# Performance work log

Hardware: AMD Instinct MI355X
Metric: run time of the kernel (lower is better)

## Reference

```python
import jax, jax.numpy as jnp
import numpy as np

NDET = 16
N_UP = 8  # spin_split=2 with nelec=16 -> (8, 8)


def _orbitals(s, r, W, b, pi, a):
    """FermiNet orbital layer for one spin.

    s: (B, n, d) backflow stream, r: (B, n, nion, 3) electron-ion displacements,
    W: (d, n*NDET), b: (n*NDET,), pi/a: (nion, n*NDET).
    Returns (NDET, B, n, n) square orbital matrices.
    """
    lin = s @ W + b                                   # (B, n, n*NDET)
    dist = jnp.linalg.norm(r, axis=-1)                # (B, n, nion)
    # isotropic envelope: sum_ion pi[ion, orb] * exp(-a[ion, orb] * |r - R_ion|)
    env = jnp.sum(pi * jnp.exp(-a * dist[..., None]), axis=-2)  # (B, n, n*NDET)
    orb = lin * env
    n = orb.shape[-2]
    orb = orb.reshape(*orb.shape[:-1], NDET, n)       # (B, n, NDET, n)
    return jnp.moveaxis(orb, -2, 0)                   # (NDET, B, n, n)


def setup_inputs() -> dict:
    key = jax.random.key(0)
    ks = jax.random.split(key, 10)
    B, NE, D, NION = 4096, 16, 256, 4
    no = N_UP * NDET
    sc = 1.0 / np.sqrt(D)
    return {
        "stream_1e": jax.random.normal(ks[0], (B, NE, D), jnp.float32),
        "r_ei": jax.random.normal(ks[1], (B, NE, NION, 3), jnp.float32),
        "W_up": jax.random.normal(ks[2], (D, no), jnp.float32) * sc,
        "b_up": jax.random.normal(ks[3], (no,), jnp.float32) * 0.01,
        "pi_up": jax.random.normal(ks[4], (NION, no), jnp.float32),
        "a_up": jax.random.uniform(ks[5], (NION, no), jnp.float32, 0.5, 1.5),
        "W_dn": jax.random.normal(ks[6], (D, no), jnp.float32) * sc,
        "b_dn": jax.random.normal(ks[7], (no,), jnp.float32) * 0.01,
        "pi_dn": jax.random.normal(ks[8], (NION, no), jnp.float32),
        "a_dn": jax.random.uniform(ks[9], (NION, no), jnp.float32, 0.5, 1.5),
    }


def reference(stream_1e, r_ei, W_up, b_up, pi_up, a_up, W_dn, b_dn, pi_dn, a_dn):
    s_up, s_dn = stream_1e[:, :N_UP], stream_1e[:, N_UP:]
    r_up, r_dn = r_ei[:, :N_UP], r_ei[:, N_UP:]
    orb_u = _orbitals(s_up, r_up, W_up, b_up, pi_up, a_up)  # (NDET, B, 8, 8)
    orb_d = _orbitals(s_dn, r_dn, W_dn, b_dn, pi_dn, a_dn)
    sgn_u, log_u = jnp.linalg.slogdet(orb_u)                # (NDET, B)
    sgn_d, log_d = jnp.linalg.slogdet(orb_d)
    sign = sgn_u * sgn_d
    logd = log_u + log_d
    # psi = sum_i det_u_i * det_d_i  (PARALLEL_EVEN, determinant_fn=None)
    m = jnp.max(logd, axis=0)                               # (B,)
    ssum = jnp.sum(sign * jnp.exp(logd - m), axis=0)        # (B,)
    log_psi = m + jnp.log(jnp.abs(ssum))                    # (B,)
    return log_psi
```

## Files before the change

kernel.cpp:

```cpp
#include <hip/hip_runtime.h>
#include <math.h>

#define DD 256
#define NO 128
#define ORW 132
#define ORB_WAVE (32*ORW)
#define UNI_US 33792
#define BUF_US 16384

typedef __attribute__((ext_vector_type(8))) short bf16x8;
typedef __attribute__((ext_vector_type(4))) float f32x4;

static __device__ inline unsigned short f2bf(float x) {
    unsigned int u = __float_as_uint(x);
    unsigned int r = (u + 0x7FFFu + ((u >> 16) & 1u)) >> 16;
    return (unsigned short)r;
}
static __device__ inline float bf2f(unsigned short h) {
    return __uint_as_float(((unsigned int)h) << 16);
}

static __device__ __forceinline__ void gl_lds16(const void* g, void* l) {
    __builtin_amdgcn_global_load_lds(
        (const __attribute__((address_space(1))) void*)g,
        (__attribute__((address_space(3))) void*)l, 16, 0, 0);
}

__global__ void prep_wt3(const float* __restrict__ Wu, const float* __restrict__ Wd,
                         unsigned short* __restrict__ wt3) {
    const int n    = blockIdx.x & 127;
    const int spin = blockIdx.x >> 7;
    const float* W = spin ? Wd : Wu;
    const int t = threadIdx.x;
    for (int k = t; k < DD; k += 64) {
        const float x = W[(size_t)k * NO + n];
        const unsigned short h = f2bf(x);
        const unsigned short l = f2bf(x - bf2f(h));
        const int kt = k >> 5, slot = (k >> 3) & 3, j = k & 7;
        const int rh = spin * 128 + n;
        const int rl = 256 + rh;
        wt3[(size_t)kt * 16384 + rh * 32 + ((slot + rh) & 3) * 8 + j] = h;
        wt3[(size_t)kt * 16384 + rl * 32 + ((slot + rl) & 3) * 8 + j] = l;
    }
}

__global__ __launch_bounds__(256, 2)
void fermi_main(const float* __restrict__ stream1e, const float* __restrict__ r_ei,
                const float* __restrict__ bu, const float* __restrict__ piu,
                const float* __restrict__ au, const float* __restrict__ bd,
                const float* __restrict__ pid_, const float* __restrict__ ad,
                const unsigned short* __restrict__ wt, float* __restrict__ out)
{
    __shared__ __align__(16) unsigned short uni[UNI_US];
    __shared__ __align__(16) float distL[4 * 32 * 4];
    __shared__ float exL[2 * 8 * 16 * 2];

    float* orb = (float*)uni;

    const int t    = threadIdx.x;
    const int w    = t >> 6;
    const int lane = t & 63;
    const int lr   = lane & 15;
    const int lg   = lane >> 4;
    const int sp   = w >> 1;
    const int bh   = w & 1;
    const int b0   = blockIdx.x * 8;

    #pragma unroll
    for (int i = 0; i < 2; ++i) {
        const int idx = lane * 2 + i;
        const int row = idx >> 2, ion = idx & 3;
        const int b  = b0 + bh * 4 + (row >> 3);
        const int ge = sp * 8 + (row & 7);
        const float* rp = r_ei + (((size_t)b * 16 + ge) * 4 + ion) * 3;
        const float x = rp[0], y = rp[1], z = rp[2];
        distL[(w * 32 + row) * 4 + ion] = sqrtf(x * x + y * y + z * z);
    }

    size_t arow0, arow1;
    {
        const int r0 = lr;
        const int r1 = 16 + lr;
        arow0 = (((size_t)(b0 + bh * 4 + (r0 >> 3)) * 16) + sp * 8 + (r0 & 7)) * DD;
        arow1 = (((size_t)(b0 + bh * 4 + (r1 >> 3)) * 16) + sp * 8 + (r1 & 7)) * DD;
    }

    auto stage = [&](int buf, int kt) {
        const unsigned short* gsrc = wt + (size_t)kt * 16384 + w * 4096 + lane * 8;
        unsigned short* ldst = uni + buf * BUF_US + w * 4096;
        #pragma unroll
        for (int i = 0; i < 8; ++i)
            gl_lds16(gsrc + i * 512, ldst + i * 512);
    };

    f32x4 acc[2][8];
    #pragma unroll
    for (int mt = 0; mt < 2; ++mt)
        #pragma unroll
        for (int nt = 0; nt < 8; ++nt)
            acc[mt][nt] = (f32x4){0.f, 0.f, 0.f, 0.f};

    stage(0, 0);
    __syncthreads();

    #pragma unroll
    for (int kt = 0; kt < 8; ++kt) {
        const int cur = kt & 1;
        if (kt < 7) stage(cur ^ 1, kt + 1);

        const int k0 = kt * 32;
        bf16x8 ah[2], al[2];
        #pragma unroll
        for (int mt = 0; mt < 2; ++mt) {
            const float* ap = stream1e + (mt ? arow1 : arow0) + k0 + lg * 8;
            const float4 v0 = *(const float4*)ap;
            const float4 v1 = *(const float4*)(ap + 4);
            const float f[8] = {v0.x, v0.y, v0.z, v0.w, v1.x, v1.y, v1.z, v1.w};
            int hw[4], lw[4];
            #pragma unroll
            for (int p = 0; p < 4; ++p) {
                unsigned int hp;
                asm("v_cvt_pk_bf16_f32 %0, %1, %2" : "=v"(hp) : "v"(f[2*p]), "v"(f[2*p+1]));
                const float h0 = __uint_as_float(hp << 16);
                const float h1 = __uint_as_float(hp & 0xFFFF0000u);
                const float l0 = f[2*p]   - h0;
                const float l1 = f[2*p+1] - h1;
                unsigned int lp;
                asm("v_cvt_pk_bf16_f32 %0, %1, %2" : "=v"(lp) : "v"(l0), "v"(l1));
                hw[p] = (int)hp;
                lw[p] = (int)lp;
            }
            ah[mt] = *(const bf16x8*)hw;
            al[mt] = *(const bf16x8*)lw;
        }
        const unsigned short* bufp = uni + cur * BUF_US;
        const int rot = ((lg + lr) & 3) * 8;
        #pragma unroll
        for (int nt = 0; nt < 8; ++nt) {
            const int rhi = sp * 128 + nt * 16 + lr;
            const bf16x8 bh_ = *(const bf16x8*)(bufp + rhi * 32 + rot);
            const bf16x8 bl_ = *(const bf16x8*)(bufp + 8192 + rhi * 32 + rot);
            acc[0][nt] = __builtin_amdgcn_mfma_f32_16x16x32_bf16(ah[0], bh_, acc[0][nt], 0, 0, 0);
            acc[0][nt] = __builtin_amdgcn_mfma_f32_16x16x32_bf16(ah[0], bl_, acc[0][nt], 0, 0, 0);
            acc[0][nt] = __builtin_amdgcn_mfma_f32_16x16x32_bf16(al[0], bh_, acc[0][nt], 0, 0, 0);
            acc[1][nt] = __builtin_amdgcn_mfma_f32_16x16x32_bf16(ah[1], bh_, acc[1][nt], 0, 0, 0);
            acc[1][nt] = __builtin_amdgcn_mfma_f32_16x16x32_bf16(ah[1], bl_, acc[1][nt], 0, 0, 0);
            acc[1][nt] = __builtin_amdgcn_mfma_f32_16x16x32_bf16(al[1], bh_, acc[1][nt], 0, 0, 0);
        }
        __syncthreads();
    }

    const float* pi_s = sp ? pid_ : piu;
    const float* a_s  = sp ? ad   : au;
    const float* b_s  = sp ? bd   : bu;
    float* ow = orb + (size_t)w * ORB_WAVE;
    {
        float dq[2][4][4];
        #pragma unroll
        for (int mt = 0; mt < 2; ++mt)
            #pragma unroll
            for (int q = 0; q < 4; ++q) {
                const int row = mt * 16 + lg * 4 + q;
                const f32x4 dv = *(const f32x4*)&distL[(w * 32 + row) * 4];
                dq[mt][q][0] = dv[0]; dq[mt][q][1] = dv[1];
                dq[mt][q][2] = dv[2]; dq[mt][q][3] = dv[3];
            }
        #pragma unroll
        for (int nt = 0; nt < 8; ++nt) {
            const int C = nt * 16 + lr;
            float pv[4], av[4];
            #pragma unroll
            for (int ion = 0; ion < 4; ++ion) {
                pv[ion] = pi_s[ion * NO + C];
                av[ion] = a_s [ion * NO + C];
            }
            const float bias = b_s[C];
            #pragma unroll
            for (int mt = 0; mt < 2; ++mt)
                #pragma unroll
                for (int q = 0; q < 4; ++q) {
                    float env = 0.f;
                    #pragma unroll
                    for (int ion = 0; ion < 4; ++ion)
                        env += pv[ion] * __expf(-av[ion] * dq[mt][q][ion]);
                    ow[(mt * 16 + lg * 4 + q) * ORW + C] = (acc[mt][nt][q] + bias) * env;
                }
        }
    }

    {
        const int bl_ = lane >> 4;
        const int dd  = lane & 15;
        const int rot = (lane >> 2) & 7;
        float M[8][8];
        #pragma unroll
        for (int j = 0; j < 8; ++j) {
            const int e = (j + rot) & 7;
            const float* pr = ow + (bl_ * 8 + e) * ORW + dd * 8;
            const f32x4 u0 = *(const f32x4*)pr;
            const f32x4 u1 = *(const f32x4*)(pr + 4);
            M[j][0] = u0[0]; M[j][1] = u0[1]; M[j][2] = u0[2]; M[j][3] = u0[3];
            M[j][4] = u1[0]; M[j][5] = u1[1]; M[j][6] = u1[2]; M[j][7] = u1[3];
        }
        float ldet = 0.f, sgn = (rot & 1) ? -1.f : 1.f;
        #pragma unroll
        for (int c = 0; c < 8; ++c) {
            #pragma unroll
            for (int r = c + 1; r < 8; ++r) {
                const bool swp = fabsf(M[r][c]) > fabsf(M[c][c]);
                sgn = swp ? -sgn : sgn;
                #pragma unroll
                for (int j = c; j < 8; ++j) {
                    const float x1 = M[c][j], x2 = M[r][j];
                    M[c][j] = swp ? x2 : x1;
                    M[r][j] = swp ? x1 : x2;
                }
            }
            const float p = M[c][c];
            ldet += __logf(fabsf(p));
            sgn  = (p < 0.f) ? -sgn : sgn;
            const float rp = (p != 0.f) ? (1.0f / p) : 0.f;
            #pragma unroll
            for (int r = c + 1; r < 8; ++r) {
                const float fm = M[r][c] * rp;
                #pragma unroll
                for (int j = c + 1; j < 8; ++j)
                    M[r][j] = fmaf(-fm, M[c][j], M[r][j]);
            }
        }
        const int bb = bh * 4 + bl_;
        exL[((sp * 8 + bb) * 16 + dd) * 2 + 0] = ldet;
        exL[((sp * 8 + bb) * 16 + dd) * 2 + 1] = sgn;
    }
    __syncthreads();

    if (t < 128) {
        const int b  = t >> 4;
        const int d2 = t & 15;
        const float lu  = exL[((b)     * 16 + d2) * 2 + 0];
        const float su  = exL[((b)     * 16 + d2) * 2 + 1];
        const float ldn = exL[((8 + b) * 16 + d2) * 2 + 0];
        const float sdn = exL[((8 + b) * 16 + d2) * 2 + 1];
        const float l   = lu + ldn;
        const float s   = su * sdn;
        float m = l;
        #pragma unroll
        for (int off = 1; off <= 8; off <<= 1) m = fmaxf(m, __shfl_xor(m, off));
        float ss = s * __expf(l - m);
        #pragma unroll
        for (int off = 1; off <= 8; off <<= 1) ss += __shfl_xor(ss, off);
        if (d2 == 0) out[b0 + b] = m + __logf(fabsf(ss));
    }
}

extern "C" void kernel_launch(void* const* d_in, const int* in_sizes, int n_in,
                              void* d_out, int out_size, void* d_ws, size_t ws_size,
                              hipStream_t stream) {
    (void)n_in; (void)in_sizes; (void)ws_size;
    const float* s1e  = (const float*)d_in[0];
    const float* r_ei = (const float*)d_in[1];
    const float* Wu   = (const float*)d_in[2];
    const float* bu   = (const float*)d_in[3];
    const float* piu  = (const float*)d_in[4];
    const float* au   = (const float*)d_in[5];
    const float* Wd   = (const float*)d_in[6];
    const float* bd   = (const float*)d_in[7];
    const float* pid_ = (const float*)d_in[8];
    const float* ad   = (const float*)d_in[9];
    float* out = (float*)d_out;
    unsigned short* wt3 = (unsigned short*)d_ws;

    hipLaunchKernelGGL(prep_wt3, dim3(256), dim3(64), 0, stream, Wu, Wd, wt3);

    const int B = out_size;
    hipLaunchKernelGGL(fermi_main, dim3(B / 8), dim3(256), 0, stream,
                       s1e, r_ei, bu, piu, au, bd, pid_, ad, wt3, out);
}
```

Before: 37.09 us.

## Split fused kernel into GEMM/envelope kernel and separate determinant kernel

Splits the single fused kernel in two. The first kernel does the bf16-split GEMM and envelope and writes the orbital matrices to a global workspace. The second kernel loads them and runs the 8x8 LU slogdet and logsumexp reduction. This removes the large LDS orbital staging buffer, which could raise occupancy of the GEMM kernel and ease register pressure. In exchange it adds a global write and read of about 32 MB of orbitals plus an extra launch.

Result: slower. 42.43 us (+14.4%).

```diff
diff --git a/kernel.cpp b/kernel.cpp
--- a/kernel.cpp
+++ b/kernel.cpp
@@ -3,10 +3,8 @@
 
 #define DD 256
 #define NO 128
-#define ORW 132
-#define ORB_WAVE (32*ORW)
-#define UNI_US 33792
 #define BUF_US 16384
+#define ORB_OFF (1u << 20)
 
 typedef __attribute__((ext_vector_type(8))) short bf16x8;
 typedef __attribute__((ext_vector_type(4))) float f32x4;
@@ -45,17 +43,14 @@
 }
 
 __global__ __launch_bounds__(256, 2)
-void fermi_main(const float* __restrict__ stream1e, const float* __restrict__ r_ei,
+void fermi_gemm(const float* __restrict__ stream1e, const float* __restrict__ r_ei,
                 const float* __restrict__ bu, const float* __restrict__ piu,
                 const float* __restrict__ au, const float* __restrict__ bd,
                 const float* __restrict__ pid_, const float* __restrict__ ad,
-                const unsigned short* __restrict__ wt, float* __restrict__ out)
+                const unsigned short* __restrict__ wt, float* __restrict__ orb_g)
 {
-    __shared__ __align__(16) unsigned short uni[UNI_US];
+    __shared__ __align__(16) unsigned short uni[2 * BUF_US];
     __shared__ __align__(16) float distL[4 * 32 * 4];
-    __shared__ float exL[2 * 8 * 16 * 2];
-
-    float* orb = (float*)uni;
 
     const int t    = threadIdx.x;
     const int w    = t >> 6;
@@ -153,7 +148,6 @@
     const float* pi_s = sp ? pid_ : piu;
     const float* a_s  = sp ? ad   : au;
     const float* b_s  = sp ? bd   : bu;
-    float* ow = orb + (size_t)w * ORB_WAVE;
     {
         float dq[2][4][4];
         #pragma unroll
@@ -179,59 +173,68 @@
             for (int mt = 0; mt < 2; ++mt)
                 #pragma unroll
                 for (int q = 0; q < 4; ++q) {
+                    const int row = mt * 16 + lg * 4 + q;
+                    const int b   = b0 + bh * 4 + (row >> 3);
+                    const int ge  = sp * 8 + (row & 7);
                     float env = 0.f;
                     #pragma unroll
                     for (int ion = 0; ion < 4; ++ion)
                         env += pv[ion] * __expf(-av[ion] * dq[mt][q][ion]);
-                    ow[(mt * 16 + lg * 4 + q) * ORW + C] = (acc[mt][nt][q] + bias) * env;
+                    orb_g[((size_t)b * 16 + ge) * NO + C] = (acc[mt][nt][q] + bias) * env;
                 }
         }
     }
-
-    {
-        const int bl_ = lane >> 4;
-        const int dd  = lane & 15;
-        const int rot = (lane >> 2) & 7;
-        float M[8][8];
-        #pragma unroll
-        for (int j = 0; j < 8; ++j) {
-            const int e = (j + rot) & 7;
-            const float* pr = ow + (bl_ * 8 + e) * ORW + dd * 8;
-            const f32x4 u0 = *(const f32x4*)pr;
-            const f32x4 u1 = *(const f32x4*)(pr + 4);
-            M[j][0] = u0[0]; M[j][1] = u0[1]; M[j][2] = u0[2]; M[j][3] = u0[3];
-            M[j][4] = u1[0]; M[j][5] = u1[1]; M[j][6] = u1[2]; M[j][7] = u1[3];
-        }
-        float ldet = 0.f, sgn = (rot & 1) ? -1.f : 1.f;
-        #pragma unroll
-        for (int c = 0; c < 8; ++c) {
-            #pragma unroll
-            for (int r = c + 1; r < 8; ++r) {
-                const bool swp = fabsf(M[r][c]) > fabsf(M[c][c]);
-                sgn = swp ? -sgn : sgn;
-                #pragma unroll
-                for (int j = c; j < 8; ++j) {
-                    const float x1 = M[c][j], x2 = M[r][j];
-                    M[c][j] = swp ? x2 : x1;
-                    M[r][j] = swp ? x1 : x2;
-                }
-            }
-            const float p = M[c][c];
-            ldet += __logf(fabsf(p));
-            sgn  = (p < 0.f) ? -sgn : sgn;
-            const float rp = (p != 0.f) ? (1.0f / p) : 0.f;
-            #pragma unroll
-            for (int r = c + 1; r < 8; ++r) {
-                const float fm = M[r][c] * rp;
-                #pragma unroll
-                for (int j = c + 1; j < 8; ++j)
-                    M[r][j] = fmaf(-fm, M[c][j], M[r][j]);
-            }
-        }
-        const int bb = bh * 4 + bl_;
-        exL[((sp * 8 + bb) * 16 + dd) * 2 + 0] = ldet;
-        exL[((sp * 8 + bb) * 16 + dd) * 2 + 1] = sgn;
-    }
+}
+
+__global__ __launch_bounds__(256)
+void fermi_det(const float* __restrict__ orb_g, float* __restrict__ out)
+{
+    __shared__ float exL[2 * 8 * 16 * 2];
+
+    const int t  = threadIdx.x;
+    const int b0 = blockIdx.x * 8;
+    const int bb = t >> 5;
+    const int sub = t & 31;
+    const int sp = sub >> 4;
+    const int dd = sub & 15;
+
+    const float* base = orb_g + (((size_t)(b0 + bb) * 16) + sp * 8) * NO + dd * 8;
+    float M[8][8];
+    #pragma unroll
+    for (int e = 0; e < 8; ++e) {
+        const f32x4 u0 = *(const f32x4*)(base + e * NO);
+        const f32x4 u1 = *(const f32x4*)(base + e * NO + 4);
+        M[e][0] = u0[0]; M[e][1] = u0[1]; M[e][2] = u0[2]; M[e][3] = u0[3];
+        M[e][4] = u1[0]; M[e][5] = u1[1]; M[e][6] = u1[2]; M[e][7] = u1[3];
+    }
+    float ldet = 0.f, sgn = 1.f;
+    #pragma unroll
+    for (int c = 0; c < 8; ++c) {
+        #pragma unroll
+        for (int r = c + 1; r < 8; ++r) {
+            const bool swp = fabsf(M[r][c]) > fabsf(M[c][c]);
+            sgn = swp ? -sgn : sgn;
+            #pragma unroll
+            for (int j = c; j < 8; ++j) {
+                const float x1 = M[c][j], x2 = M[r][j];
+                M[c][j] = swp ? x2 : x1;
+                M[r][j] = swp ? x1 : x2;
+            }
+        }
+        const float p = M[c][c];
+        ldet += __logf(fabsf(p));
+        sgn  = (p < 0.f) ? -sgn : sgn;
+        const float rp = (p != 0.f) ? (1.0f / p) : 0.f;
+        #pragma unroll
+        for (int r = c + 1; r < 8; ++r) {
+            const float fm = M[r][c] * rp;
+            #pragma unroll
+            for (int j = c + 1; j < 8; ++j)
+                M[r][j] = fmaf(-fm, M[c][j], M[r][j]);
+        }
+    }
+    exL[((sp * 8 + bb) * 16 + dd) * 2 + 0] = ldet;
+    exL[((sp * 8 + bb) * 16 + dd) * 2 + 1] = sgn;
     __syncthreads();
 
     if (t < 128) {
@@ -269,10 +272,12 @@
     const float* ad   = (const float*)d_in[9];
     float* out = (float*)d_out;
     unsigned short* wt3 = (unsigned short*)d_ws;
+    float* orb_g = (float*)d_ws + ORB_OFF;
 
     hipLaunchKernelGGL(prep_wt3, dim3(256), dim3(64), 0, stream, Wu, Wd, wt3);
 
     const int B = out_size;
-    hipLaunchKernelGGL(fermi_main, dim3(B / 8), dim3(256), 0, stream,
-                       s1e, r_ei, bu, piu, au, bd, pid_, ad, wt3, out);
-}
+    hipLaunchKernelGGL(fermi_gemm, dim3(B / 8), dim3(256), 0, stream,
+                       s1e, r_ei, bu, piu, au, bd, pid_, ad, wt3, orb_g);
+    hipLaunchKernelGGL(fermi_det, dim3(B / 8), dim3(256), 0, stream, orb_g, out);
+}
```

## Triple-buffer hi weight tiles, read lo weights from global, prefetch activations

Applied to the files above, without the earlier changes.

Only the high-bf16 weight half is staged into LDS now, using a three-deep ring with counted vmcnt waits and raw barriers in place of a full double buffer with __syncthreads. The low-bf16 half is laid out in fragment order and loaded straight from global memory. Activation rows for the next k-step are prefetched into registers one iteration ahead, and MFMA priority is raised around the compute loop. The aim is to shrink LDS traffic and hide load latency, at the cost of more direct global/L2 reads and tight vmcnt bookkeeping that must match the number of loads in flight.

Result: slower. 40.47 us (+9.1%).

```diff
diff --git a/kernel.cpp b/kernel.cpp
--- a/kernel.cpp
+++ b/kernel.cpp
@@ -6,7 +6,8 @@
 #define ORW 132
 #define ORB_WAVE (32*ORW)
 #define UNI_US 33792
-#define BUF_US 16384
+#define TILE_US 8192
+#define LO_OFF 65536
 
 typedef __attribute__((ext_vector_type(8))) short bf16x8;
 typedef __attribute__((ext_vector_type(4))) float f32x4;
@@ -26,21 +27,22 @@
         (__attribute__((address_space(3))) void*)l, 16, 0, 0);
 }
 
-__global__ void prep_wt3(const float* __restrict__ Wu, const float* __restrict__ Wd,
-                         unsigned short* __restrict__ wt3) {
+__global__ void prep_wt4(const float* __restrict__ Wu, const float* __restrict__ Wd,
+                         unsigned short* __restrict__ wt4) {
     const int n    = blockIdx.x & 127;
     const int spin = blockIdx.x >> 7;
     const float* W = spin ? Wd : Wu;
     const int t = threadIdx.x;
+    const int nt = n >> 4, lr = n & 15;
     for (int k = t; k < DD; k += 64) {
         const float x = W[(size_t)k * NO + n];
         const unsigned short h = f2bf(x);
         const unsigned short l = f2bf(x - bf2f(h));
         const int kt = k >> 5, slot = (k >> 3) & 3, j = k & 7;
-        const int rh = spin * 128 + n;
-        const int rl = 256 + rh;
-        wt3[(size_t)kt * 16384 + rh * 32 + ((slot + rh) & 3) * 8 + j] = h;
-        wt3[(size_t)kt * 16384 + rl * 32 + ((slot + rl) & 3) * 8 + j] = l;
+        const int row = spin * 128 + n;
+        wt4[(size_t)kt * TILE_US + row * 32 + ((slot + row) & 3) * 8 + j] = h;
+        wt4[(size_t)LO_OFF + ((size_t)(spin * 8 + kt) * 8 + nt) * 512
+            + (slot * 16 + lr) * 8 + j] = l;
     }
 }
 
@@ -86,10 +88,10 @@
     }
 
     auto stage = [&](int buf, int kt) {
-        const unsigned short* gsrc = wt + (size_t)kt * 16384 + w * 4096 + lane * 8;
-        unsigned short* ldst = uni + buf * BUF_US + w * 4096;
-        #pragma unroll
-        for (int i = 0; i < 8; ++i)
+        const unsigned short* gsrc = wt + (size_t)kt * TILE_US + w * 2048 + lane * 8;
+        unsigned short* ldst = uni + buf * TILE_US + w * 2048;
+        #pragma unroll
+        for (int i = 0; i < 4; ++i)
             gl_lds16(gsrc + i * 512, ldst + i * 512);
     };
 
@@ -101,21 +103,36 @@
             acc[mt][nt] = (f32x4){0.f, 0.f, 0.f, 0.f};
 
     stage(0, 0);
-    __syncthreads();
-
+    stage(1, 1);
+    float4 aq[2][2];
     #pragma unroll
-    for (int kt = 0; kt < 8; ++kt) {
-        const int cur = kt & 1;
-        if (kt < 7) stage(cur ^ 1, kt + 1);
-
-        const int k0 = kt * 32;
+    for (int mt = 0; mt < 2; ++mt) {
+        const float* ap = stream1e + (mt ? arow1 : arow0) + lg * 8;
+        aq[mt][0] = *(const float4*)ap;
+        aq[mt][1] = *(const float4*)(ap + 4);
+    }
+    asm volatile("s_waitcnt vmcnt(8)" ::: "memory");
+    __builtin_amdgcn_s_barrier();
+    __builtin_amdgcn_sched_barrier(0);
+
+    #pragma unroll
+    for (int kt2 = 0; kt2 < 8; ++kt2) {
+        if (kt2 < 6) stage((kt2 + 2) % 3, kt2 + 2);
+        float4 an[2][2];
+        if (kt2 < 7) {
+            const int k0n = (kt2 + 1) * 32;
+            #pragma unroll
+            for (int mt = 0; mt < 2; ++mt) {
+                const float* ap = stream1e + (mt ? arow1 : arow0) + k0n + lg * 8;
+                an[mt][0] = *(const float4*)ap;
+                an[mt][1] = *(const float4*)(ap + 4);
+            }
+        }
         bf16x8 ah[2], al[2];
         #pragma unroll
         for (int mt = 0; mt < 2; ++mt) {
-            const float* ap = stream1e + (mt ? arow1 : arow0) + k0 + lg * 8;
-            const float4 v0 = *(const float4*)ap;
-            const float4 v1 = *(const float4*)(ap + 4);
-            const float f[8] = {v0.x, v0.y, v0.z, v0.w, v1.x, v1.y, v1.z, v1.w};
+            const float f[8] = {aq[mt][0].x, aq[mt][0].y, aq[mt][0].z, aq[mt][0].w,
+                                aq[mt][1].x, aq[mt][1].y, aq[mt][1].z, aq[mt][1].w};
             int hw[4], lw[4];
             #pragma unroll
             for (int p = 0; p < 4; ++p) {
@@ -133,22 +150,37 @@
             ah[mt] = *(const bf16x8*)hw;
             al[mt] = *(const bf16x8*)lw;
         }
-        const unsigned short* bufp = uni + cur * BUF_US;
+        const unsigned short* bufp = uni + (kt2 % 3) * TILE_US;
+        const unsigned short* lop  = wt + LO_OFF
+                                   + ((size_t)(sp * 8 + kt2) * 8) * 512 + lane * 8;
         const int rot = ((lg + lr) & 3) * 8;
+        __builtin_amdgcn_s_setprio(1);
         #pragma unroll
         for (int nt = 0; nt < 8; ++nt) {
-            const int rhi = sp * 128 + nt * 16 + lr;
-            const bf16x8 bh_ = *(const bf16x8*)(bufp + rhi * 32 + rot);
-            const bf16x8 bl_ = *(const bf16x8*)(bufp + 8192 + rhi * 32 + rot);
+            const int row = sp * 128 + nt * 16 + lr;
+            const bf16x8 bh_ = *(const bf16x8*)(bufp + row * 32 + rot);
+            const bf16x8 bl_ = *(const bf16x8*)(lop + nt * 512);
             acc[0][nt] = __builtin_amdgcn_mfma_f32_16x16x32_bf16(ah[0], bh_, acc[0][nt], 0, 0, 0);
+            acc[0][nt] = __builtin_amdgcn_mfma_f32_16x16x32_bf16(al[0], bh_, acc[0][nt], 0, 0, 0);
             acc[0][nt] = __builtin_amdgcn_mfma_f32_16x16x32_bf16(ah[0], bl_, acc[0][nt], 0, 0, 0);
-            acc[0][nt] = __builtin_amdgcn_mfma_f32_16x16x32_bf16(al[0], bh_, acc[0][nt], 0, 0, 0);
             acc[1][nt] = __builtin_amdgcn_mfma_f32_16x16x32_bf16(ah[1], bh_, acc[1][nt], 0, 0, 0);
+            acc[1][nt] = __builtin_amdgcn_mfma_f32_16x16x32_bf16(al[1], bh_, acc[1][nt], 0, 0, 0);
             acc[1][nt] = __builtin_amdgcn_mfma_f32_16x16x32_bf16(ah[1], bl_, acc[1][nt], 0, 0, 0);
-            acc[1][nt] = __builtin_amdgcn_mfma_f32_16x16x32_bf16(al[1], bh_, acc[1][nt], 0, 0, 0);
-        }
-        __syncthreads();
-    }
+        }
+        __builtin_amdgcn_s_setprio(0);
+        if (kt2 < 7) {
+            if (kt2 < 6) asm volatile("s_waitcnt vmcnt(8)" ::: "memory");
+            else         asm volatile("s_waitcnt vmcnt(4)" ::: "memory");
+            __builtin_amdgcn_s_barrier();
+            __builtin_amdgcn_sched_barrier(0);
+            #pragma unroll
+            for (int mt = 0; mt < 2; ++mt) {
+                aq[mt][0] = an[mt][0];
+                aq[mt][1] = an[mt][1];
+            }
+        }
+    }
+    __syncthreads();
 
     const float* pi_s = sp ? pid_ : piu;
     const float* a_s  = sp ? ad   : au;
@@ -268,11 +300,11 @@
     const float* pid_ = (const float*)d_in[8];
     const float* ad   = (const float*)d_in[9];
     float* out = (float*)d_out;
-    unsigned short* wt3 = (unsigned short*)d_ws;
-
-    hipLaunchKernelGGL(prep_wt3, dim3(256), dim3(64), 0, stream, Wu, Wd, wt3);
+    unsigned short* wt4 = (unsigned short*)d_ws;
+
+    hipLaunchKernelGGL(prep_wt4, dim3(256), dim3(64), 0, stream, Wu, Wd, wt4);
 
     const int B = out_size;
     hipLaunchKernelGGL(fermi_main, dim3(B / 8), dim3(256), 0, stream,
-                       s1e, r_ei, bu, piu, au, bd, pid_, ad, wt3, out);
-}
+                       s1e, r_ei, bu, piu, au, bd, pid_, ad, wt4, out);
+}
```
